# Optimization experiments

Measured on AMD Instinct MI355X. Metric: run time of the kernel, lower is better.

The kernel has to match this reference:

```python
import jax, jax.numpy as jnp
import numpy as np

B, L, D = 4, 2048, 1024
E, F, H = 6, 1536, 512  # experts, d_ff, router hidden
TOP_K = 2
LN_EPS = 1e-5

def setup_inputs() -> dict:
    key = jax.random.key(0)
    ks = jax.random.split(key, 8)
    s = lambda fan: 1.0 / np.sqrt(fan)
    return {
        "x": jax.random.normal(ks[0], (B, L, D), jnp.float32),
        "r1_w": jax.random.normal(ks[1], (D, H), jnp.float32) * s(D),
        "r1_b": jnp.zeros((H,), jnp.float32),
        "ln_g": jnp.ones((H,), jnp.float32),
        "ln_b": jnp.zeros((H,), jnp.float32),
        "r2_w": jax.random.normal(ks[2], (H, E), jnp.float32) * s(H),
        "r2_b": jnp.zeros((E,), jnp.float32),
        "temp": jnp.ones((1,), jnp.float32),
        "route_bias": jnp.zeros((E,), jnp.float32),
        "W1": jax.random.normal(ks[3], (E, D, F), jnp.float32) * s(D),
        "b1": jnp.zeros((E, F), jnp.float32),
        "W2": jax.random.normal(ks[4], (E, F, D), jnp.float32) * s(F),
        "b2": jnp.zeros((E, D), jnp.float32),
    }

def reference(x, r1_w, r1_b, ln_g, ln_b, r2_w, r2_b, temp, route_bias, W1, b1, W2, b2):
    b, l, d = x.shape
    xf = x.reshape(-1, d)                       # [N, D]
    n = xf.shape[0]
    # Router: Linear -> LayerNorm -> GELU(exact) -> Linear
    h = xf @ r1_w + r1_b                        # [N, H]
    mu = jnp.mean(h, axis=-1, keepdims=True)
    var = jnp.mean((h - mu) ** 2, axis=-1, keepdims=True)
    h = (h - mu) * jax.lax.rsqrt(var + LN_EPS) * ln_g + ln_b
    h = jax.nn.gelu(h, approximate=False)
    logits = (h @ r2_w + r2_b) / temp + route_bias   # [N, E]
    p = jax.nn.softmax(logits, axis=-1)
    top_v, top_i = jax.lax.top_k(p, TOP_K)      # [N, k]
    probs = jnp.zeros_like(p).at[jnp.arange(n)[:, None], top_i].set(top_v)  # [N, E]
    # Dense all-expert MLPs (faithful to source, which computes every expert)
    hh = jnp.einsum('nd,edf->enf', xf, W1) + b1[:, None, :]   # [E, N, F]
    even = (jnp.arange(W1.shape[0]) % 2 == 0)[:, None, None]
    act = jnp.where(even, jax.nn.gelu(hh, approximate=False), jax.nn.silu(hh))
    eo = jnp.einsum('enf,efd->end', act, W2) + b2[:, None, :]  # [E, N, D]
    out = jnp.einsum('ne,end->nd', probs, eo)   # weighted combine
    return out.reshape(b, l, d)
```

## Files before the change

### kernel.cpp

```cpp
#include <hip/hip_runtime.h>
#include <hip/hip_bf16.h>
#include <stdint.h>

typedef __bf16 bf16;
typedef bf16 bf16x8 __attribute__((ext_vector_type(8)));
typedef bf16 bf16x4 __attribute__((ext_vector_type(4)));
typedef float f32x4 __attribute__((ext_vector_type(4)));
typedef int i32x4 __attribute__((ext_vector_type(4)));

#define N_TOK 8192
#define D_MODEL 1024
#define H_R 512
#define N_EXP 6
#define F_FF 1536
#define FLAG_CAP 1024

__device__ __forceinline__ float erf_fast(float x) {
    float ax = fabsf(x);
    float t = 1.0f / (1.0f + 0.3275911f * ax);
    float p = t * (0.254829592f + t * (-0.284496736f + t * (1.421413741f +
              t * (-1.453152027f + t * 1.061405429f))));
    float r = 1.0f - p * __expf(-ax * ax);
    return copysignf(r, x);
}
__device__ __forceinline__ float gelu_f(float x) {
    return 0.5f * x * (1.0f + erf_fast(x * 0.70710678118654752f));
}
__device__ __forceinline__ float silu_f(float x) {
    return x * (1.0f / (1.0f + __expf(-x)));
}

typedef __attribute__((address_space(1))) const void* gas1;
typedef __attribute__((address_space(3))) void* las3;

__device__ __forceinline__ void gload16(const void* g, void* l) {
    __builtin_amdgcn_global_load_lds((gas1)g, (las3)l, 16, 0, 0);
}

__device__ __forceinline__ int swz_src_q(int c) {
    return (((c & 3) - ((c >> 2) >> 1)) & 3);
}

#define GATE(N) asm volatile("s_waitcnt vmcnt(" #N ")\n\ts_barrier" ::: "memory")


__global__ __launch_bounds__(256) void convert_x_split(
    const float* __restrict__ x, bf16* __restrict__ xh, bf16* __restrict__ xl) {
    size_t i = ((size_t)blockIdx.x * 256 + threadIdx.x) * 8;
    f32x4 a = *(const f32x4*)(x + i);
    f32x4 b = *(const f32x4*)(x + i + 4);
    float v[8] = {a[0], a[1], a[2], a[3], b[0], b[1], b[2], b[3]};
    bf16x8 vh, vl;
    #pragma unroll
    for (int k = 0; k < 8; ++k) {
        bf16 h = (bf16)v[k];
        vh[k] = h;
        vl[k] = (bf16)(v[k] - (float)h);
    }
    *(bf16x8*)(xh + i) = vh;
    *(bf16x8*)(xl + i) = vl;
}

__global__ __launch_bounds__(256) void transpose_bf16_64(
    const float* __restrict__ in, bf16* __restrict__ out, int R, int C) {
    __shared__ float tile[64][65];
    const float* inp = in + (size_t)blockIdx.z * R * C;
    bf16* op = out + (size_t)blockIdx.z * R * C;
    int tx = threadIdx.x & 15, ty = threadIdx.x >> 4;
    int r0 = blockIdx.y * 64, c0 = blockIdx.x * 64;
    #pragma unroll
    for (int p = 0; p < 4; ++p) {
        int row = p * 16 + ty;
        f32x4 v = *(const f32x4*)(inp + (size_t)(r0 + row) * C + c0 + tx * 4);
        tile[row][tx * 4 + 0] = v[0];
        tile[row][tx * 4 + 1] = v[1];
        tile[row][tx * 4 + 2] = v[2];
        tile[row][tx * 4 + 3] = v[3];
    }
    __syncthreads();
    #pragma unroll
    for (int p = 0; p < 4; ++p) {
        int cc = p * 16 + ty;
        bf16x4 o;
        #pragma unroll
        for (int k = 0; k < 4; ++k) o[k] = (bf16)tile[tx * 4 + k][cc];
        *(bf16x4*)(op + (size_t)(c0 + cc) * R + r0 + tx * 4) = o;
    }
}

__global__ __launch_bounds__(256) void transpose_split(
    const float* __restrict__ in, bf16* __restrict__ oh, bf16* __restrict__ ol,
    int R, int C) {
    __shared__ float tile[32][33];
    int tx = threadIdx.x & 31, ty = threadIdx.x >> 5;
    int r0 = blockIdx.y * 32, c0 = blockIdx.x * 32;
    #pragma unroll
    for (int yy = ty; yy < 32; yy += 8)
        tile[yy][tx] = in[(size_t)(r0 + yy) * C + c0 + tx];
    __syncthreads();
    #pragma unroll
    for (int yy = ty; yy < 32; yy += 8) {
        float v = tile[tx][yy];
        bf16 h = (bf16)v;
        size_t o = (size_t)(c0 + yy) * R + r0 + tx;
        oh[o] = h;
        ol[o] = (bf16)(v - (float)h);
    }
}


__device__ __forceinline__ void gemm128_core(
    const bf16* gA0, const bf16* gA1, const bf16* gB0, const bf16* gB1,
    int K, bf16* sm, f32x4 acc[4][4])
{
    const int tid = threadIdx.x;
    const int lane = tid & 63;
    const int w = tid >> 6;
    const int wm = w & 1, wn = w >> 1;
    const int lc = lane & 15;
    const int koff = ((((lane >> 4) + (lc >> 1)) & 3) * 8);
    const int ws = w * 512;
    const int NT = K >> 5;
    gload16(gA0,      sm + ws);
    gload16(gA1,      sm + 2048 + ws);
    gload16(gB0,      sm + 4096 + ws);
    gload16(gB1,      sm + 6144 + ws);
    gload16(gA0 + 32, sm + 8192 + ws);
    gload16(gA1 + 32, sm + 8192 + 2048 + ws);
    gload16(gB0 + 32, sm + 8192 + 4096 + ws);
    gload16(gB1 + 32, sm + 8192 + 6144 + ws);
    int cur = 0, nxt = 8192, fut = 16384;
    for (int t = 0; t < NT; ++t) {
        if (t + 2 < NT) {
            const int kb = (t + 2) << 5;
            gload16(gA0 + kb, sm + fut + ws);
            gload16(gA1 + kb, sm + fut + 2048 + ws);
            gload16(gB0 + kb, sm + fut + 4096 + ws);
            gload16(gB1 + kb, sm + fut + 6144 + ws);
            GATE(8);
        } else if (t + 1 < NT) {
            GATE(4);
        } else {
            GATE(0);
        }
        bf16x8 af[4], bfr[4];
        #pragma unroll
        for (int i = 0; i < 4; ++i)
            af[i] = *(const bf16x8*)(sm + cur + (wm * 64 + i * 16 + lc) * 32 + koff);
        #pragma unroll
        for (int j = 0; j < 4; ++j)
            bfr[j] = *(const bf16x8*)(sm + cur + 4096 + (wn * 64 + j * 16 + lc) * 32 + koff);
        __builtin_amdgcn_s_barrier();
        __builtin_amdgcn_s_setprio(1);
        #pragma unroll
        for (int i = 0; i < 4; ++i)
            #pragma unroll
            for (int j = 0; j < 4; ++j)
                acc[i][j] = __builtin_amdgcn_mfma_f32_16x16x32_bf16(af[i], bfr[j], acc[i][j], 0, 0, 0);
        __builtin_amdgcn_s_setprio(0);
        int old = cur; cur = nxt; nxt = fut; fut = old;
    }
}


__global__ __launch_bounds__(256, 2) void router_gemm_fused(
    const bf16* __restrict__ xh, const bf16* __restrict__ xl,
    const bf16* __restrict__ wTh, const bf16* __restrict__ wTl,
    float* __restrict__ hp) {
    __shared__ bf16 smem[32768];
    const int tid = threadIdx.x;
    const int mbase = blockIdx.y * 128, nbase = blockIdx.x * 128;
    const int c0 = tid, c1 = tid + 256;
    const size_t ra0 = (size_t)(mbase + (c0 >> 2)) * D_MODEL + swz_src_q(c0) * 8;
    const size_t ra1 = (size_t)(mbase + (c1 >> 2)) * D_MODEL + swz_src_q(c1) * 8;
    const size_t rb0 = (size_t)(nbase + (c0 >> 2)) * D_MODEL + swz_src_q(c0) * 8;
    const size_t rb1 = (size_t)(nbase + (c1 >> 2)) * D_MODEL + swz_src_q(c1) * 8;
    const bf16 *pxh0 = xh + ra0, *pxh1 = xh + ra1;
    const bf16 *pxl0 = xl + ra0, *pxl1 = xl + ra1;
    const bf16 *pwh0 = wTh + rb0, *pwh1 = wTh + rb1;
    const bf16 *pwl0 = wTl + rb0, *pwl1 = wTl + rb1;
    const int w = tid >> 6, lane = tid & 63;
    const int wm = w & 1, wn = w >> 1, lc = lane & 15;
    const int koff = ((((lane >> 4) + (lc >> 1)) & 3) * 8);
    const int ws = w * 512;
    f32x4 acc[4][4] = {};
    gload16(pxh0, smem + ws);
    gload16(pxh1, smem + 2048 + ws);
    gload16(pxl0, smem + 4096 + ws);
    gload16(pxl1, smem + 6144 + ws);
    gload16(pwh0, smem + 8192 + ws);
    gload16(pwh1, smem + 10240 + ws);
    gload16(pwl0, smem + 12288 + ws);
    gload16(pwl1, smem + 14336 + ws);
    int bo = 0;
    for (int t = 0; t < D_MODEL / 32; ++t) {
        const int nb = bo ^ 16384;
        if (t + 1 < D_MODEL / 32) {
            const int kb = (t + 1) << 5;
            gload16(pxh0 + kb, smem + nb + ws);
            gload16(pxh1 + kb, smem + nb + 2048 + ws);
            gload16(pxl0 + kb, smem + nb + 4096 + ws);
            gload16(pxl1 + kb, smem + nb + 6144 + ws);
            gload16(pwh0 + kb, smem + nb + 8192 + ws);
            gload16(pwh1 + kb, smem + nb + 10240 + ws);
            gload16(pwl0 + kb, smem + nb + 12288 + ws);
            gload16(pwl1 + kb, smem + nb + 14336 + ws);
            GATE(8);
        } else {
            GATE(0);
        }
        bf16x8 ah[4], al[4], bh[4], bl[4];
        #pragma unroll
        for (int i = 0; i < 4; ++i) {
            const int ro = (wm * 64 + i * 16 + lc) * 32 + koff;
            ah[i] = *(const bf16x8*)(smem + bo + ro);
            al[i] = *(const bf16x8*)(smem + bo + 4096 + ro);
        }
        #pragma unroll
        for (int j = 0; j < 4; ++j) {
            const int ro = (wn * 64 + j * 16 + lc) * 32 + koff;
            bh[j] = *(const bf16x8*)(smem + bo + 8192 + ro);
            bl[j] = *(const bf16x8*)(smem + bo + 12288 + ro);
        }
        __builtin_amdgcn_s_barrier();
        __builtin_amdgcn_s_setprio(1);
        #pragma unroll
        for (int i = 0; i < 4; ++i)
            #pragma unroll
            for (int j = 0; j < 4; ++j) {
                acc[i][j] = __builtin_amdgcn_mfma_f32_16x16x32_bf16(ah[i], bh[j], acc[i][j], 0, 0, 0);
                acc[i][j] = __builtin_amdgcn_mfma_f32_16x16x32_bf16(ah[i], bl[j], acc[i][j], 0, 0, 0);
                acc[i][j] = __builtin_amdgcn_mfma_f32_16x16x32_bf16(al[i], bh[j], acc[i][j], 0, 0, 0);
            }
        __builtin_amdgcn_s_setprio(0);
        bo = nb;
    }
    const int quad = lane >> 4;
    #pragma unroll
    for (int i = 0; i < 4; ++i)
        #pragma unroll
        for (int j = 0; j < 4; ++j) {
            int col = nbase + wn * 64 + j * 16 + lc;
            #pragma unroll
            for (int r = 0; r < 4; ++r) {
                int row = mbase + wm * 64 + i * 16 + quad * 4 + r;
                hp[(size_t)row * H_R + col] = acc[i][j][r];
            }
        }
}


__global__ __launch_bounds__(256) void ln_router2(
    const float* __restrict__ hp, const float* __restrict__ r1b,
    const float* __restrict__ g, const float* __restrict__ bta,
    const float* __restrict__ r2w, const float* __restrict__ r2b,
    const float* __restrict__ temp, const float* __restrict__ rbias,
    int* __restrict__ top_i, float* __restrict__ top_p,
    int* __restrict__ flaglist, int* __restrict__ meta) {
    __shared__ float Wl[H_R * N_EXP];
    int tid = threadIdx.x;
    for (int i = tid; i < H_R * N_EXP; i += 256) Wl[i] = r2w[i];
    __syncthreads();
    int w = tid >> 6, lane = tid & 63;
    int t = blockIdx.x * 4 + w;
    size_t rbase = (size_t)t * H_R;
    int k0 = lane * 8;
    float v[8];
    {
        f32x4 a0 = *(const f32x4*)(hp + rbase + k0);
        f32x4 a1 = *(const f32x4*)(hp + rbase + k0 + 4);
        f32x4 d0 = *(const f32x4*)(r1b + k0);
        f32x4 d1 = *(const f32x4*)(r1b + k0 + 4);
        #pragma unroll
        for (int k = 0; k < 4; ++k) {
            v[k]     = a0[k] + d0[k];
            v[k + 4] = a1[k] + d1[k];
        }
    }
    float s = 0.f;
    #pragma unroll
    for (int k = 0; k < 8; ++k) s += v[k];
    #pragma unroll
    for (int off = 32; off; off >>= 1) s += __shfl_xor(s, off);
    float mu = s * (1.0f / H_R);
    float q = 0.f;
    #pragma unroll
    for (int k = 0; k < 8; ++k) { float d = v[k] - mu; q += d * d; }
    #pragma unroll
    for (int off = 32; off; off >>= 1) q += __shfl_xor(q, off);
    float scl = 1.0f / sqrtf(q * (1.0f / H_R) + 1e-5f);
    f32x4 g0 = *(const f32x4*)(g + k0), g1 = *(const f32x4*)(g + k0 + 4);
    f32x4 b0 = *(const f32x4*)(bta + k0), b1v = *(const f32x4*)(bta + k0 + 4);
    float G[8] = {g0[0], g0[1], g0[2], g0[3], g1[0], g1[1], g1[2], g1[3]};
    float B[8] = {b0[0], b0[1], b0[2], b0[3], b1v[0], b1v[1], b1v[2], b1v[3]};
    float acc[N_EXP] = {};
    #pragma unroll
    for (int k = 0; k < 8; ++k) {
        float y = gelu_f((v[k] - mu) * scl * G[k] + B[k]);
        const float* wr = &Wl[(k0 + k) * N_EXP];
        #pragma unroll
        for (int e = 0; e < N_EXP; ++e) acc[e] += y * wr[e];
    }
    #pragma unroll
    for (int e = 0; e < N_EXP; ++e)
        #pragma unroll
        for (int off = 32; off; off >>= 1) acc[e] += __shfl_xor(acc[e], off);
    if (lane == 0) {
        float tinv = 1.0f / temp[0];
        float lg[N_EXP];
        #pragma unroll
        for (int e = 0; e < N_EXP; ++e) lg[e] = (acc[e] + r2b[e]) * tinv + rbias[e];
        float v1 = -1e30f; int i1 = 0;
        #pragma unroll
        for (int e = 0; e < N_EXP; ++e) if (lg[e] > v1) { v1 = lg[e]; i1 = e; }
        float v2 = -1e30f; int i2 = 0;
        #pragma unroll
        for (int e = 0; e < N_EXP; ++e) if (e != i1 && lg[e] > v2) { v2 = lg[e]; i2 = e; }
        float v3 = -1e30f;
        #pragma unroll
        for (int e = 0; e < N_EXP; ++e) if (e != i1 && e != i2 && lg[e] > v3) v3 = lg[e];
        float ssum = 0.f;
        #pragma unroll
        for (int e = 0; e < N_EXP; ++e) ssum += __expf(lg[e] - v1);
        float inv = 1.0f / ssum;
        top_i[2 * t] = i1; top_i[2 * t + 1] = i2;
        top_p[2 * t] = inv;
        top_p[2 * t + 1] = __expf(v2 - v1) * inv;
        if (v2 - v3 < 1e-3f) {
            int ix = atomicAdd(&meta[24], 1);
            if (ix < FLAG_CAP) flaglist[ix] = t;
        }
    }
}


__global__ __launch_bounds__(256) void router_rescue(
    const float* __restrict__ x, const float* __restrict__ r1w,
    const float* __restrict__ r1b, const float* __restrict__ lng,
    const float* __restrict__ lnb, const float* __restrict__ r2w,
    const float* __restrict__ r2b, const float* __restrict__ temp,
    const float* __restrict__ rbias, const int* __restrict__ flaglist,
    const int* __restrict__ meta, int* __restrict__ top_i, float* __restrict__ top_p) {
    int n = meta[24]; if (n > FLAG_CAP) n = FLAG_CAP;
    if ((int)blockIdx.x >= n) return;
    int t = flaglist[blockIdx.x];
    __shared__ double xs[D_MODEL];
    __shared__ double hbuf[H_R];
    __shared__ double red[8];
    int tid = threadIdx.x;
    for (int k = tid; k < D_MODEL; k += 256) xs[k] = (double)x[(size_t)t * D_MODEL + k];
    __syncthreads();
    for (int c = tid; c < H_R; c += 256) {
        double s = 0.0;
        for (int k = 0; k < D_MODEL; ++k) s += xs[k] * (double)r1w[(size_t)k * H_R + c];
        hbuf[c] = s + (double)r1b[c];
    }
    __syncthreads();
    double ls = 0.0;
    for (int c = tid; c < H_R; c += 256) ls += hbuf[c];
    #pragma unroll
    for (int off = 32; off; off >>= 1) ls += __shfl_xor(ls, off);
    if ((tid & 63) == 0) red[tid >> 6] = ls;
    __syncthreads();
    double mu = (red[0] + red[1] + red[2] + red[3]) * (1.0 / H_R);
    __syncthreads();
    double q = 0.0;
    for (int c = tid; c < H_R; c += 256) { double d = hbuf[c] - mu; q += d * d; }
    #pragma unroll
    for (int off = 32; off; off >>= 1) q += __shfl_xor(q, off);
    if ((tid & 63) == 0) red[tid >> 6] = q;
    __syncthreads();
    double var = (red[0] + red[1] + red[2] + red[3]) * (1.0 / H_R);
    double scl = 1.0 / sqrt(var + 1e-5);
    __syncthreads();
    for (int c = tid; c < H_R; c += 256) {
        double y = (hbuf[c] - mu) * scl * (double)lng[c] + (double)lnb[c];
        hbuf[c] = 0.5 * y * (1.0 + erf(y * 0.70710678118654752440));
    }
    __syncthreads();
    if (tid < N_EXP) {
        double s = 0.0;
        for (int k = 0; k < H_R; ++k) s += hbuf[k] * (double)r2w[k * N_EXP + tid];
        red[tid] = (s + (double)r2b[tid]) / (double)temp[0] + (double)rbias[tid];
    }
    __syncthreads();
    if (tid == 0) {
        double lg[N_EXP];
        #pragma unroll
        for (int e = 0; e < N_EXP; ++e) lg[e] = red[e];
        double v1 = -1e300; int i1 = 0;
        for (int e = 0; e < N_EXP; ++e) if (lg[e] > v1) { v1 = lg[e]; i1 = e; }
        double v2 = -1e300; int i2 = 0;
        for (int e = 0; e < N_EXP; ++e) if (e != i1 && lg[e] > v2) { v2 = lg[e]; i2 = e; }
        double s = 0.0;
        for (int e = 0; e < N_EXP; ++e) s += exp(lg[e] - v1);
        double inv = 1.0 / s;
        top_i[2 * t] = i1; top_i[2 * t + 1] = i2;
        top_p[2 * t] = (float)inv;
        top_p[2 * t + 1] = (float)(exp(v2 - v1) * inv);
    }
}


#define RP_T 1024
#define RP_TOK (N_TOK / RP_T)

__global__ __launch_bounds__(1024) void route_pack(
    const int* __restrict__ top_i, int* __restrict__ meta,
    int* __restrict__ atok, int* __restrict__ ainv) {
    __shared__ int S[N_EXP][RP_T];
    __shared__ int segbase[N_EXP + 1];
    int tid = threadIdx.x;
    int e_loc[2 * RP_TOK];
    int cnt[N_EXP];
    #pragma unroll
    for (int e = 0; e < N_EXP; ++e) cnt[e] = 0;
    int t0 = tid * RP_TOK;
    #pragma unroll
    for (int q = 0; q < (2 * RP_TOK) / 4; ++q) {
        i32x4 v = *(const i32x4*)(top_i + 2 * t0 + q * 4);
        #pragma unroll
        for (int k = 0; k < 4; ++k) {
            int e = v[k];
            e_loc[q * 4 + k] = e;
            #pragma unroll
            for (int ee = 0; ee < N_EXP; ++ee) if (e == ee) cnt[ee]++;
        }
    }
    #pragma unroll
    for (int e = 0; e < N_EXP; ++e) S[e][tid] = cnt[e];
    __syncthreads();
    for (int off = 1; off < RP_T; off <<= 1) {
        int tmp[N_EXP];
        #pragma unroll
        for (int e = 0; e < N_EXP; ++e)
            tmp[e] = (tid >= off) ? S[e][tid - off] : 0;
        __syncthreads();
        #pragma unroll
        for (int e = 0; e < N_EXP; ++e) S[e][tid] += tmp[e];
        __syncthreads();
    }
    if (tid == 0) {
        int o = 0;
        #pragma unroll
        for (int e = 0; e < N_EXP; ++e) {
            segbase[e] = o;
            int tot = S[e][RP_T - 1];
            meta[e] = tot;
            meta[8 + e] = o;
            o += tot;
        }
        segbase[N_EXP] = o;
    }
    __syncthreads();
    int pos[N_EXP];
    #pragma unroll
    for (int e = 0; e < N_EXP; ++e)
        pos[e] = segbase[e] + S[e][tid] - cnt[e];
    #pragma unroll
    for (int k = 0; k < 2 * RP_TOK; ++k) {
        int e = e_loc[k];
        int a = 0;
        #pragma unroll
        for (int ee = 0; ee < N_EXP; ++ee) if (e == ee) a = pos[ee]++;
        atok[a] = t0 + (k >> 1);
        ainv[2 * t0 + k] = a;
    }
}


#define NX1 (F_FF / 128)
#define NX2 (D_MODEL / 128)

__global__ __launch_bounds__(256, 3) void expert_gemm1(
    const bf16* __restrict__ xb, const bf16* __restrict__ W1T,
    const float* __restrict__ b1, const int* __restrict__ meta,
    const int* __restrict__ atok, bf16* __restrict__ act) {
    __shared__ bf16 smem[24576];
    const int id = blockIdx.x;
    const int xcd = id & 7, slot = id >> 3;
    const int xt = slot % NX1;
    const int g = (slot / NX1) * 8 + xcd;
    const int e = g % N_EXP, y = g / N_EXP;
    int rows = meta[e];
    int mloc = y * 128;
    if (mloc >= rows) return;
    int base = meta[8 + e];
    int tid = threadIdx.x;
    int nbase = xt * 128;
    int c0 = tid, c1 = tid + 256;
    int r0 = mloc + (c0 >> 2); if (r0 > rows - 1) r0 = rows - 1;
    int r1 = mloc + (c1 >> 2); if (r1 > rows - 1) r1 = rows - 1;
    const bf16* gA0 = xb + (size_t)atok[base + r0] * D_MODEL + swz_src_q(c0) * 8;
    const bf16* gA1 = xb + (size_t)atok[base + r1] * D_MODEL + swz_src_q(c1) * 8;
    const bf16* Bt = W1T + ((size_t)e * F_FF + nbase) * D_MODEL;
    const bf16* gB0 = Bt + (size_t)(c0 >> 2) * D_MODEL + swz_src_q(c0) * 8;
    const bf16* gB1 = Bt + (size_t)(c1 >> 2) * D_MODEL + swz_src_q(c1) * 8;
    f32x4 acc[4][4] = {};
    gemm128_core(gA0, gA1, gB0, gB1, D_MODEL, smem, acc);
    const int lane = tid & 63;
    const int w = tid >> 6;
    const int wm = w & 1, wn = w >> 1;
    const int lc = lane & 15, qd = lane >> 4;
    const bool oddE = (e & 1) != 0;
    #pragma unroll
    for (int i = 0; i < 4; ++i) {
        #pragma unroll
        for (int j = 0; j < 4; ++j) {
            int col = nbase + wn * 64 + j * 16 + lc;
            float bias = b1[e * F_FF + col];
            #pragma unroll
            for (int r = 0; r < 4; ++r) {
                int rloc = mloc + wm * 64 + i * 16 + qd * 4 + r;
                if (rloc < rows) {
                    float vv = acc[i][j][r] + bias;
                    vv = oddE ? silu_f(vv) : gelu_f(vv);
                    act[(size_t)(base + rloc) * F_FF + col] = (bf16)vv;
                }
            }
        }
    }
}

__global__ __launch_bounds__(256, 3) void expert_gemm2(
    const bf16* __restrict__ act, const bf16* __restrict__ W2T,
    const float* __restrict__ b2, const int* __restrict__ meta,
    float* __restrict__ eo) {
    __shared__ bf16 smem[24576];
    const int id = blockIdx.x;
    const int xcd = id & 7, slot = id >> 3;
    const int xt = slot % NX2;
    const int g = (slot / NX2) * 8 + xcd;
    const int e = g % N_EXP, y = g / N_EXP;
    int rows = meta[e];
    int mloc = y * 128;
    if (mloc >= rows) return;
    int base = meta[8 + e];
    int tid = threadIdx.x;
    int nbase = xt * 128;
    int c0 = tid, c1 = tid + 256;
    int r0 = mloc + (c0 >> 2); if (r0 > rows - 1) r0 = rows - 1;
    int r1 = mloc + (c1 >> 2); if (r1 > rows - 1) r1 = rows - 1;
    const bf16* gA0 = act + (size_t)(base + r0) * F_FF + swz_src_q(c0) * 8;
    const bf16* gA1 = act + (size_t)(base + r1) * F_FF + swz_src_q(c1) * 8;
    const bf16* Bt = W2T + ((size_t)e * D_MODEL + nbase) * F_FF;
    const bf16* gB0 = Bt + (size_t)(c0 >> 2) * F_FF + swz_src_q(c0) * 8;
    const bf16* gB1 = Bt + (size_t)(c1 >> 2) * F_FF + swz_src_q(c1) * 8;
    f32x4 acc[4][4] = {};
    gemm128_core(gA0, gA1, gB0, gB1, F_FF, smem, acc);
    const int lane = tid & 63;
    const int w = tid >> 6;
    const int wm = w & 1, wn = w >> 1;
    const int lc = lane & 15, qd = lane >> 4;
    #pragma unroll
    for (int i = 0; i < 4; ++i) {
        #pragma unroll
        for (int j = 0; j < 4; ++j) {
            int col = nbase + wn * 64 + j * 16 + lc;
            float bias = b2[e * D_MODEL + col];
            #pragma unroll
            for (int r = 0; r < 4; ++r) {
                int rloc = mloc + wm * 64 + i * 16 + qd * 4 + r;
                if (rloc < rows)
                    eo[(size_t)(base + rloc) * D_MODEL + col] = acc[i][j][r] + bias;
            }
        }
    }
}


__global__ __launch_bounds__(256) void combine_kernel(
    const float* __restrict__ eo, const int* __restrict__ ainv,
    const float* __restrict__ top_p, float* __restrict__ out) {
    int t = blockIdx.x;
    int s0 = ainv[2 * t], s1 = ainv[2 * t + 1];
    float p0 = top_p[2 * t], p1 = top_p[2 * t + 1];
    int c = threadIdx.x * 4;
    f32x4 a = *(const f32x4*)(eo + (size_t)s0 * D_MODEL + c);
    f32x4 b = *(const f32x4*)(eo + (size_t)s1 * D_MODEL + c);
    f32x4 o;
    #pragma unroll
    for (int k = 0; k < 4; ++k) o[k] = a[k] * p0 + b[k] * p1;
    *(f32x4*)(out + (size_t)t * D_MODEL + c) = o;
}


extern "C" void kernel_launch(void* const* d_in, const int* in_sizes, int n_in,
                              void* d_out, int out_size, void* d_ws, size_t ws_size,
                              hipStream_t stream) {
    const float* x     = (const float*)d_in[0];
    const float* r1w   = (const float*)d_in[1];
    const float* r1b   = (const float*)d_in[2];
    const float* lng   = (const float*)d_in[3];
    const float* lnb   = (const float*)d_in[4];
    const float* r2w   = (const float*)d_in[5];
    const float* r2b   = (const float*)d_in[6];
    const float* temp  = (const float*)d_in[7];
    const float* rbias = (const float*)d_in[8];
    const float* W1    = (const float*)d_in[9];
    const float* b1    = (const float*)d_in[10];
    const float* W2    = (const float*)d_in[11];
    const float* b2    = (const float*)d_in[12];
    float* out = (float*)d_out;

    char* ws = (char*)d_ws;
    size_t off = 0;
    auto alloc = [&](size_t bytes) -> void* {
        void* p = ws + off;
        off = (off + bytes + 255) & ~(size_t)255;
        return p;
    };
    bf16*  xh    = (bf16*)alloc((size_t)N_TOK * D_MODEL * 2);
    bf16*  xl    = (bf16*)alloc((size_t)N_TOK * D_MODEL * 2);
    bf16*  r1wTh = (bf16*)alloc((size_t)H_R * D_MODEL * 2);
    bf16*  r1wTl = (bf16*)alloc((size_t)H_R * D_MODEL * 2);
    bf16*  W1T   = (bf16*)alloc((size_t)N_EXP * F_FF * D_MODEL * 2);
    bf16*  W2T   = (bf16*)alloc((size_t)N_EXP * D_MODEL * F_FF * 2);
    float* hp    = (float*)alloc((size_t)N_TOK * H_R * 4);
    int*   top_i = (int*)alloc((size_t)N_TOK * 2 * 4);
    float* top_p = (float*)alloc((size_t)N_TOK * 2 * 4);
    int*   meta  = (int*)alloc(256);
    int*   flags = (int*)alloc(FLAG_CAP * 4);
    int*   atok  = (int*)alloc((size_t)2 * N_TOK * 4);
    int*   ainv  = (int*)alloc((size_t)2 * N_TOK * 4);
    bf16*  actb  = (bf16*)alloc((size_t)2 * N_TOK * F_FF * 2);
    float* eo    = (float*)alloc((size_t)2 * N_TOK * D_MODEL * 4);
    (void)ws_size; (void)n_in; (void)in_sizes;

    hipMemsetAsync(meta, 0, 256, stream);

    convert_x_split<<<(N_TOK * D_MODEL) / (256 * 8), 256, 0, stream>>>(x, xh, xl);
    transpose_split<<<dim3(H_R / 32, D_MODEL / 32, 1), 256, 0, stream>>>(
        r1w, r1wTh, r1wTl, D_MODEL, H_R);

    router_gemm_fused<<<dim3(H_R / 128, N_TOK / 128, 1), 256, 0, stream>>>(
        xh, xl, r1wTh, r1wTl, hp);
    ln_router2<<<N_TOK / 4, 256, 0, stream>>>(
        hp, r1b, lng, lnb, r2w, r2b, temp, rbias, top_i, top_p, flags, meta);
    router_rescue<<<FLAG_CAP, 256, 0, stream>>>(
        x, r1w, r1b, lng, lnb, r2w, r2b, temp, rbias, flags, meta, top_i, top_p);
    route_pack<<<1, RP_T, 0, stream>>>(top_i, meta, atok, ainv);

    transpose_bf16_64<<<dim3(F_FF / 64, D_MODEL / 64, N_EXP), 256, 0, stream>>>(
        W1, W1T, D_MODEL, F_FF);
    transpose_bf16_64<<<dim3(D_MODEL / 64, F_FF / 64, N_EXP), 256, 0, stream>>>(
        W2, W2T, F_FF, D_MODEL);

    expert_gemm1<<<(N_TOK / 128) * N_EXP * NX1, 256, 0, stream>>>(
        xh, W1T, b1, meta, atok, actb);
    expert_gemm2<<<(N_TOK / 128) * N_EXP * NX2, 256, 0, stream>>>(
        actb, W2T, b2, meta, eo);
    combine_kernel<<<N_TOK, 256, 0, stream>>>(eo, ainv, top_p, out);
}
```

Before: 524.1 us.

## Fuse weighted combine into expert GEMM2 via atomics and compact tile table

Removes the separate combine kernel and the fp32 expert-output buffer. GEMM2 now scales each row by its routing weight and atomically adds it into a pre-zeroed output. Expert GEMM launches now index a compact table of only the non-empty 128-row tiles, built in route_pack, instead of launching a grid sized for the worst case and exiting empty blocks early. The cost is a memset of the output, fp32 atomic traffic with contention on rows that receive two experts, and summation order that is no longer deterministic.

Measured after the change: 551.0 us. 1.05x slower.

```diff
diff --git a/kernel.cpp b/kernel.cpp
--- a/kernel.cpp
+++ b/kernel.cpp
@@ -14,6 +14,7 @@
 #define N_EXP 6
 #define F_FF 1536
 #define FLAG_CAP 1024
+#define PMAX 17
 
 __device__ __forceinline__ float erf_fast(float x) {
     float ax = fabsf(x);
@@ -406,8 +407,9 @@
 #define RP_TOK (N_TOK / RP_T)
 
 __global__ __launch_bounds__(1024) void route_pack(
-    const int* __restrict__ top_i, int* __restrict__ meta,
-    int* __restrict__ atok, int* __restrict__ ainv) {
+    const int* __restrict__ top_i, const float* __restrict__ top_p,
+    int* __restrict__ meta, int* __restrict__ atok, float* __restrict__ pw,
+    int* __restrict__ ptab) {
     __shared__ int S[N_EXP][RP_T];
     __shared__ int segbase[N_EXP + 1];
     int tid = threadIdx.x;
@@ -442,6 +444,7 @@
     }
     if (tid == 0) {
         int o = 0;
+        int tp = 0;
         #pragma unroll
         for (int e = 0; e < N_EXP; ++e) {
             segbase[e] = o;
@@ -449,8 +452,11 @@
             meta[e] = tot;
             meta[8 + e] = o;
             o += tot;
+            int np = (tot + 127) >> 7;
+            for (int y = 0; y < np; ++y) ptab[tp++] = e | (y << 8);
         }
         segbase[N_EXP] = o;
+        meta[16] = tp;
     }
     __syncthreads();
     int pos[N_EXP];
@@ -464,7 +470,7 @@
         #pragma unroll
         for (int ee = 0; ee < N_EXP; ++ee) if (e == ee) a = pos[ee]++;
         atok[a] = t0 + (k >> 1);
-        ainv[2 * t0 + k] = a;
+        pw[a] = top_p[2 * t0 + k];
     }
 }
 
@@ -475,16 +481,20 @@
 __global__ __launch_bounds__(256, 3) void expert_gemm1(
     const bf16* __restrict__ xb, const bf16* __restrict__ W1T,
     const float* __restrict__ b1, const int* __restrict__ meta,
-    const int* __restrict__ atok, bf16* __restrict__ act) {
+    const int* __restrict__ atok, const int* __restrict__ ptab,
+    bf16* __restrict__ act) {
     __shared__ bf16 smem[24576];
     const int id = blockIdx.x;
     const int xcd = id & 7, slot = id >> 3;
-    const int xt = slot % NX1;
-    const int g = (slot / NX1) * 8 + xcd;
-    const int e = g % N_EXP, y = g / N_EXP;
+    const int p = slot / NX1, xt = slot % NX1;
+    const int total = meta[16];
+    const int Q = (total + 7) >> 3;
+    const int gidx = xcd * Q + p;
+    if (p >= Q || gidx >= total) return;
+    const int ent = ptab[gidx];
+    const int e = ent & 255, y = ent >> 8;
     int rows = meta[e];
     int mloc = y * 128;
-    if (mloc >= rows) return;
     int base = meta[8 + e];
     int tid = threadIdx.x;
     int nbase = xt * 128;
@@ -525,16 +535,20 @@
 __global__ __launch_bounds__(256, 3) void expert_gemm2(
     const bf16* __restrict__ act, const bf16* __restrict__ W2T,
     const float* __restrict__ b2, const int* __restrict__ meta,
-    float* __restrict__ eo) {
+    const int* __restrict__ atok, const float* __restrict__ pw,
+    const int* __restrict__ ptab, float* __restrict__ out) {
     __shared__ bf16 smem[24576];
     const int id = blockIdx.x;
     const int xcd = id & 7, slot = id >> 3;
-    const int xt = slot % NX2;
-    const int g = (slot / NX2) * 8 + xcd;
-    const int e = g % N_EXP, y = g / N_EXP;
+    const int p = slot / NX2, xt = slot % NX2;
+    const int total = meta[16];
+    const int Q = (total + 7) >> 3;
+    const int gidx = xcd * Q + p;
+    if (p >= Q || gidx >= total) return;
+    const int ent = ptab[gidx];
+    const int e = ent & 255, y = ent >> 8;
     int rows = meta[e];
     int mloc = y * 128;
-    if (mloc >= rows) return;
     int base = meta[8 + e];
     int tid = threadIdx.x;
     int nbase = xt * 128;
@@ -555,33 +569,20 @@
     #pragma unroll
     for (int i = 0; i < 4; ++i) {
         #pragma unroll
-        for (int j = 0; j < 4; ++j) {
-            int col = nbase + wn * 64 + j * 16 + lc;
-            float bias = b2[e * D_MODEL + col];
-            #pragma unroll
-            for (int r = 0; r < 4; ++r) {
-                int rloc = mloc + wm * 64 + i * 16 + qd * 4 + r;
-                if (rloc < rows)
-                    eo[(size_t)(base + rloc) * D_MODEL + col] = acc[i][j][r] + bias;
+        for (int r = 0; r < 4; ++r) {
+            int rloc = mloc + wm * 64 + i * 16 + qd * 4 + r;
+            if (rloc < rows) {
+                int token = atok[base + rloc];
+                float wgt = pw[base + rloc];
+                float* orow = out + (size_t)token * D_MODEL;
+                #pragma unroll
+                for (int j = 0; j < 4; ++j) {
+                    int col = nbase + wn * 64 + j * 16 + lc;
+                    atomicAdd(orow + col, wgt * (acc[i][j][r] + b2[e * D_MODEL + col]));
+                }
             }
         }
     }
-}
-
-
-__global__ __launch_bounds__(256) void combine_kernel(
-    const float* __restrict__ eo, const int* __restrict__ ainv,
-    const float* __restrict__ top_p, float* __restrict__ out) {
-    int t = blockIdx.x;
-    int s0 = ainv[2 * t], s1 = ainv[2 * t + 1];
-    float p0 = top_p[2 * t], p1 = top_p[2 * t + 1];
-    int c = threadIdx.x * 4;
-    f32x4 a = *(const f32x4*)(eo + (size_t)s0 * D_MODEL + c);
-    f32x4 b = *(const f32x4*)(eo + (size_t)s1 * D_MODEL + c);
-    f32x4 o;
-    #pragma unroll
-    for (int k = 0; k < 4; ++k) o[k] = a[k] * p0 + b[k] * p1;
-    *(f32x4*)(out + (size_t)t * D_MODEL + c) = o;
 }
 
 
@@ -622,12 +623,13 @@
     int*   meta  = (int*)alloc(256);
     int*   flags = (int*)alloc(FLAG_CAP * 4);
     int*   atok  = (int*)alloc((size_t)2 * N_TOK * 4);
-    int*   ainv  = (int*)alloc((size_t)2 * N_TOK * 4);
+    float* pw    = (float*)alloc((size_t)2 * N_TOK * 4);
+    int*   ptab  = (int*)alloc(1024);
     bf16*  actb  = (bf16*)alloc((size_t)2 * N_TOK * F_FF * 2);
-    float* eo    = (float*)alloc((size_t)2 * N_TOK * D_MODEL * 4);
     (void)ws_size; (void)n_in; (void)in_sizes;
 
     hipMemsetAsync(meta, 0, 256, stream);
+    hipMemsetAsync(out, 0, (size_t)N_TOK * D_MODEL * 4, stream);
 
     convert_x_split<<<(N_TOK * D_MODEL) / (256 * 8), 256, 0, stream>>>(x, xh, xl);
     transpose_split<<<dim3(H_R / 32, D_MODEL / 32, 1), 256, 0, stream>>>(
@@ -639,16 +641,15 @@
         hp, r1b, lng, lnb, r2w, r2b, temp, rbias, top_i, top_p, flags, meta);
     router_rescue<<<FLAG_CAP, 256, 0, stream>>>(
         x, r1w, r1b, lng, lnb, r2w, r2b, temp, rbias, flags, meta, top_i, top_p);
-    route_pack<<<1, RP_T, 0, stream>>>(top_i, meta, atok, ainv);
+    route_pack<<<1, RP_T, 0, stream>>>(top_i, top_p, meta, atok, pw, ptab);
 
     transpose_bf16_64<<<dim3(F_FF / 64, D_MODEL / 64, N_EXP), 256, 0, stream>>>(
         W1, W1T, D_MODEL, F_FF);
     transpose_bf16_64<<<dim3(D_MODEL / 64, F_FF / 64, N_EXP), 256, 0, stream>>>(
         W2, W2T, F_FF, D_MODEL);
 
-    expert_gemm1<<<(N_TOK / 128) * N_EXP * NX1, 256, 0, stream>>>(
-        xh, W1T, b1, meta, atok, actb);
-    expert_gemm2<<<(N_TOK / 128) * N_EXP * NX2, 256, 0, stream>>>(
-        actb, W2T, b2, meta, eo);
-    combine_kernel<<<N_TOK, 256, 0, stream>>>(eo, ainv, top_p, out);
-}
+    expert_gemm1<<<8 * PMAX * NX1, 256, 0, stream>>>(
+        xh, W1T, b1, meta, atok, ptab, actb);
+    expert_gemm2<<<8 * PMAX * NX2, 256, 0, stream>>>(
+        actb, W2T, b2, meta, atok, pw, ptab, out);
+}
```
